# Optimization experiments

Measured on AMD Instinct MI355X. Metric: run time of the kernel, lower is better.

## Reference

```python
import jax, jax.numpy as jnp
import numpy as np

NUM_TERMS = 3
HIDDEN = 64
CLAMP_MIN = 1e-10


def _hermite_basis(x, num_terms):
    hs = [jnp.ones_like(x)]
    if num_terms > 1:
        hs.append(2.0 * x)
    for n in range(1, num_terms - 1):
        hs.append(2.0 * x * hs[n] - 2.0 * n * hs[n - 1])
    return jnp.stack(hs[:num_terms], axis=-1)  # (..., num_terms)


def setup_inputs() -> dict:
    key = jax.random.key(0)
    ks = jax.random.split(key, 7)
    B, S = 2048, 1024
    ys_coeffs = jax.random.normal(ks[0], (B, S, 2), dtype=jnp.float32)
    # scoring MLP params: Linear(3,64) -> ReLU -> Linear(64,64) -> ReLU -> Linear(64,num_terms)
    def lin(k, fan_in, fan_out):
        bound = 1.0 / np.sqrt(fan_in)
        kw, kb = jax.random.split(k)
        W = jax.random.uniform(kw, (fan_in, fan_out), minval=-bound, maxval=bound, dtype=jnp.float32)
        b = jax.random.uniform(kb, (fan_out,), minval=-bound, maxval=bound, dtype=jnp.float32)
        return W, b
    W1, b1 = lin(ks[1], 3, HIDDEN)
    W2, b2 = lin(ks[2], HIDDEN, HIDDEN)
    Wout, bout = lin(ks[3], HIDDEN, NUM_TERMS)
    return {"ys_coeffs": ys_coeffs, "W1": W1, "b1": b1, "W2": W2, "b2": b2,
            "Wout": Wout, "bout": bout}


def reference(ys_coeffs, W1, b1, W2, b2, Wout, bout):
    B, S, _ = ys_coeffs.shape
    timestamps = ys_coeffs[:, :, 0]
    values = ys_coeffs[:, :, 1]
    x0 = values[:, :-1]            # (B, S-1)
    xt = values[:, 1:]             # (B, S-1)
    t = timestamps[:, 1:]          # (B, S-1)
    feats = jnp.stack([xt, t, x0], axis=-1)           # (B, S-1, 3)
    h1 = jax.nn.relu(feats @ W1 + b1)                 # (B, S-1, 64)
    h2 = jax.nn.relu(h1 @ W2 + b2)                    # (B, S-1, 64)
    c_n = h2 @ Wout + bout                            # (B, S-1, num_terms)
    herm = _hermite_basis(xt, NUM_TERMS)              # (B, S-1, num_terms)
    p = jnp.sum(c_n * herm, axis=-1)                  # (B, S-1)
    p = jax.nn.softmax(p, axis=0)                     # softmax over batch dim (as in torch dim=0)
    log_likelihood = jnp.log(jnp.clip(p, CLAMP_MIN)).sum(axis=-1)  # (B,)
    return log_likelihood.mean()
```

## Files before the change

### kernel.cpp

```cpp
#include <hip/hip_runtime.h>
#include <hip/hip_bf16.h>

#define HIDDEN 64
#define BATCH 2048
#define SFULL 1024
#define SM1 1023
#define LN_CLAMP -23.025850929940457f
#define SP_PER 16

typedef __bf16 bf16x8 __attribute__((ext_vector_type(8)));
typedef float  f32x4  __attribute__((ext_vector_type(4)));
typedef float  f32x16 __attribute__((ext_vector_type(16)));
typedef short  s16x2  __attribute__((ext_vector_type(2)));

#define FRAG_UNITS 16

__device__ __forceinline__ int sig(int rg) {
    return 16 * ((rg >> 3) & 3) + 8 * ((rg >> 2) & 1) + (rg & 3) + 4 * (rg >> 5);
}

__device__ __forceinline__ unsigned pkt(float lo, float hi) {
    return __builtin_amdgcn_perm(__float_as_uint(hi), __float_as_uint(lo), 0x07060302u);
}
__device__ __forceinline__ unsigned rp(unsigned x) {
    s16x2 v = __builtin_bit_cast(s16x2, x);
    s16x2 z = {0, 0};
    v = __builtin_elementwise_max(v, z);
    return __builtin_bit_cast(unsigned, v);
}

__device__ __forceinline__ void relu_pack4(const f32x16 lo, const f32x16 hi, bf16x8* out) {
#pragma unroll
    for (int c = 0; c < 4; ++c) {
        union { unsigned u[4]; bf16x8 v; } r;
        r.u[0] = rp(pkt(lo[4 * c + 0], lo[4 * c + 1]));
        r.u[1] = rp(pkt(lo[4 * c + 2], lo[4 * c + 3]));
        r.u[2] = rp(pkt(hi[4 * c + 0], hi[4 * c + 1]));
        r.u[3] = rp(pkt(hi[4 * c + 2], hi[4 * c + 3]));
        out[c] = r.v;
    }
}

__device__ __forceinline__ bf16x8 featpk(float xt, float t, float x0) {
    union { unsigned u[4]; bf16x8 v; } r;
    r.u[0] = pkt(xt, t);
    r.u[1] = pkt(x0, 1.0f);
    r.u[2] = r.u[0]; r.u[3] = r.u[1];
    return r.v;
}

__global__ __launch_bounds__(256) void frag_setup_kernel(
    const float* __restrict__ W1, const float* __restrict__ b1,
    const float* __restrict__ W2, const float* __restrict__ b2,
    const float* __restrict__ Wout, char* __restrict__ F)
{
    const int l    = threadIdx.x & 63;
    const int wv   = threadIdx.x >> 6;
    const int pcol = l & 31;
    const int hi   = l >> 5;

    if (wv == 0) {
#pragma unroll
        for (int mt = 0; mt < 2; ++mt) {
            const int hout = sig(32 * mt + pcol);
            bf16x8 v;
#pragma unroll
            for (int j = 0; j < 8; ++j) {
                const int k = 8 * hi + j;
                v[j] = (k < 3) ? (__bf16)W1[k * 64 + hout]
                     : (k == 3) ? (__bf16)b1[hout] : (__bf16)0.0f;
            }
            *(bf16x8*)(F + ((mt * 64 + l) << 4)) = v;
        }
#pragma unroll
        for (int c = 0; c < 4; ++c) {
            bf16x8 v;
#pragma unroll
            for (int j = 0; j < 8; ++j) {
                const int k = 16 * c + 8 * hi + j;
                v[j] = (pcol < 3) ? (__bf16)Wout[k * 3 + pcol] : (__bf16)0.0f;
            }
            *(bf16x8*)(F + (((10 + c) * 64 + l) << 4)) = v;
        }
    } else if (wv == 1 || wv == 2) {
        const int mt = wv - 1;
        const int hout = sig(32 * mt + pcol);
#pragma unroll
        for (int c = 0; c < 4; ++c) {
            bf16x8 v;
#pragma unroll
            for (int j = 0; j < 8; ++j)
                v[j] = (__bf16)W2[(16 * c + 8 * hi + j) * 64 + hout];
            *(bf16x8*)(F + (((2 + mt * 4 + c) * 64 + l) << 4)) = v;
        }
    } else {
#pragma unroll
        for (int mt = 0; mt < 2; ++mt) {
            const int hout = sig(32 * mt + pcol);
            bf16x8 v;
#pragma unroll
            for (int j = 0; j < 8; ++j)
                v[j] = (hi == 0 && j == 0) ? (__bf16)b2[hout] : (__bf16)0.0f;
            *(bf16x8*)(F + (((14 + mt) * 64 + l) << 4)) = v;
        }
    }
}

__global__ __launch_bounds__(256, 4) void mlp_z_kernel(
    const float* __restrict__ ys,
    const char* __restrict__ F,
    const float* __restrict__ bout,
    float* __restrict__ z)
{
    __shared__ __align__(16) char Flds[14 * 64 * 16];

    const int l    = threadIdx.x & 63;
    const int wv   = threadIdx.x >> 6;
    const int pcol = l & 31;
    const int hi   = l >> 5;

    for (int i = threadIdx.x; i < 14 * 64; i += 256)
        *(f32x4*)(Flds + ((size_t)i << 4)) =
            *(const f32x4*)(F + ((size_t)(2 * 64 + i) << 4));

    const int b   = (blockIdx.x * 4 + wv) * 32 + pcol;
    const int sp0 = blockIdx.y * SP_PER;
    const int omax = (SFULL - 1) - sp0;

    bf16x8 a1r[2];
    a1r[0] = *(const bf16x8*)(F + ((0 * 64 + l) << 4));
    a1r[1] = *(const bf16x8*)(F + ((1 * 64 + l) << 4));

    bf16x8 Bone;
    {
        union { unsigned u[4]; bf16x8 v; } r;
        r.u[0] = (hi == 0) ? 0x3F80u : 0u;
        r.u[1] = 0u; r.u[2] = 0u; r.u[3] = 0u;
        Bone = r.v;
    }

    const float bo0 = bout[0], bo1 = bout[1], bo2 = bout[2];

    f32x16 zero16;
#pragma unroll
    for (int i = 0; i < 16; ++i) zero16[i] = 0.0f;

    const float2* base2 = reinterpret_cast<const float2*>(ys) + ((size_t)b * SFULL + sp0);
    float* zb = z + (size_t)sp0 * BATCH + b;

    float2 q0 = base2[0];
    float2 q1 = base2[min(1, omax)];
    float2 qn = base2[min(2, omax)];

    __syncthreads();

    for (int it = 0; it < SP_PER; ++it) {
        unsigned loff = (unsigned)(l << 4);
        asm volatile("" : "+v"(loff));
#define LDSF(u) (*(const bf16x8*)(Flds + ((u) * 1024) + loff))

        const float2 qn2 = base2[min(it + 3, omax)];

        const float x0 = q0.y, t = q1.x, xt = q1.y;
        const bf16x8 f0 = featpk(xt, t, x0);

        f32x16 acc1_0 = __builtin_amdgcn_mfma_f32_32x32x16_bf16(a1r[0], f0, zero16, 0, 0, 0);
        f32x16 acc1_1 = __builtin_amdgcn_mfma_f32_32x32x16_bf16(a1r[1], f0, zero16, 0, 0, 0);

        bf16x8 wb0 = LDSF(12), wb1 = LDSF(13);
        bf16x8 w2_0 = LDSF(0), w2_1 = LDSF(4);

        bf16x8 h1f[4];
        relu_pack4(acc1_0, acc1_1, h1f);

        f32x16 acc2_0 = __builtin_amdgcn_mfma_f32_32x32x16_bf16(wb0, Bone, zero16, 0, 0, 0);
        f32x16 acc2_1 = __builtin_amdgcn_mfma_f32_32x32x16_bf16(wb1, Bone, zero16, 0, 0, 0);

#pragma unroll
        for (int c = 0; c < 4; ++c) {
            bf16x8 n0, n1;
            if (c < 3) { n0 = LDSF(c + 1); n1 = LDSF(4 + c + 1); }
            acc2_0 = __builtin_amdgcn_mfma_f32_32x32x16_bf16(w2_0, h1f[c], acc2_0, 0, 0, 0);
            acc2_1 = __builtin_amdgcn_mfma_f32_32x32x16_bf16(w2_1, h1f[c], acc2_1, 0, 0, 0);
            if (c < 3) { w2_0 = n0; w2_1 = n1; }
        }

        bf16x8 h2f[4];
        relu_pack4(acc2_0, acc2_1, h2f);

        bf16x8 w3 = LDSF(8);
        f32x16 acc3;
#pragma unroll
        for (int c = 0; c < 4; ++c) {
            bf16x8 n3;
            if (c < 3) n3 = LDSF(8 + c + 1);
            acc3 = __builtin_amdgcn_mfma_f32_32x32x16_bf16(w3, h2f[c],
                        (c == 0) ? zero16 : acc3, 0, 0, 0);
            if (c < 3) w3 = n3;
        }
#undef LDSF

        const float c0 = acc3[0] + bo0;
        const float c1 = acc3[1] + bo1;
        const float c2 = acc3[2] + bo2;
        const float zv = fmaf(c2, fmaf(4.0f * xt, xt, -2.0f), fmaf(c1, xt + xt, c0));

        if (l < 32 && sp0 + it < SM1)
            zb[(size_t)it * BATCH] = zv;

        q0 = q1; q1 = qn; qn = qn2;
    }
}

__device__ __forceinline__ float blk_reduce_max(float v) {
    __shared__ float s[4];
#pragma unroll
    for (int off = 32; off >= 1; off >>= 1) v = fmaxf(v, __shfl_xor(v, off));
    if ((threadIdx.x & 63) == 0) s[threadIdx.x >> 6] = v;
    __syncthreads();
    v = fmaxf(fmaxf(s[0], s[1]), fmaxf(s[2], s[3]));
    __syncthreads();
    return v;
}

__device__ __forceinline__ float blk_reduce_sum(float v) {
    __shared__ float s[4];
#pragma unroll
    for (int off = 32; off >= 1; off >>= 1) v += __shfl_xor(v, off);
    if ((threadIdx.x & 63) == 0) s[threadIdx.x >> 6] = v;
    __syncthreads();
    v = (s[0] + s[1]) + (s[2] + s[3]);
    __syncthreads();
    return v;
}

__global__ __launch_bounds__(256) void col_softmax_kernel(
    const float* __restrict__ z, float* __restrict__ colsum)
{
    const int sp = blockIdx.x;
    const int tid = threadIdx.x;
    const float* col = z + (size_t)sp * BATCH;

    float vals[8];
    float m = -3.4e38f;
#pragma unroll
    for (int i = 0; i < 8; ++i) {
        vals[i] = col[tid + 256 * i];
        m = fmaxf(m, vals[i]);
    }
    const float M = blk_reduce_max(m);

    float se = 0.0f;
#pragma unroll
    for (int i = 0; i < 8; ++i) se += __expf(vals[i] - M);
    const float S = blk_reduce_sum(se);
    const float L = __logf(S);

    float acc = 0.0f;
#pragma unroll
    for (int i = 0; i < 8; ++i) acc += fmaxf(vals[i] - M - L, LN_CLAMP);
    const float T = blk_reduce_sum(acc);
    if (tid == 0) colsum[sp] = T;
}

__global__ __launch_bounds__(256) void final_reduce_kernel(
    const float* __restrict__ colsum, float* __restrict__ out)
{
    const int tid = threadIdx.x;
    float v = 0.0f;
    for (int i = tid; i < SM1; i += 256) v += colsum[i];
    const float T = blk_reduce_sum(v);
    if (tid == 0) out[0] = T / (float)BATCH;
}

extern "C" void kernel_launch(void* const* d_in, const int* in_sizes, int n_in,
                              void* d_out, int out_size, void* d_ws, size_t ws_size,
                              hipStream_t stream) {
    const float* ys   = (const float*)d_in[0];
    const float* W1   = (const float*)d_in[1];
    const float* b1   = (const float*)d_in[2];
    const float* W2   = (const float*)d_in[3];
    const float* b2   = (const float*)d_in[4];
    const float* Wout = (const float*)d_in[5];
    const float* bout = (const float*)d_in[6];
    float* out = (float*)d_out;

    float* z      = (float*)d_ws;
    float* colsum = z + (size_t)SM1 * BATCH;
    size_t fo = ((size_t)SM1 * BATCH + SM1) * sizeof(float);
    fo = (fo + 15) & ~(size_t)15;
    char* F = (char*)d_ws + fo;

    frag_setup_kernel<<<1, 256, 0, stream>>>(W1, b1, W2, b2, Wout, F);
    dim3 grid1(16, 64);
    mlp_z_kernel<<<grid1, 256, 0, stream>>>(ys, F, bout, z);
    col_softmax_kernel<<<SM1, 256, 0, stream>>>(z, colsum);
    final_reduce_kernel<<<1, 256, 0, stream>>>(colsum, out);
}
```

Before: 44.17 us.

## Software-pipeline layer-1 MFMA across timesteps and split layer-3 accumulation chain

Restructures the per-timestep loop into pairs with ping-pong accumulators, so the first-layer MFMA for the next timestep is issued while the current timestep runs layers 2 and 3. Layer 3 now uses two independent accumulator chains that are summed at the end, which shortens the dependent MFMA chain. Launch bounds drop from 4 to 2 blocks per CU to make room for the extra live accumulators. This trades occupancy for instruction-level parallelism inside each wave.

```diff
diff --git a/kernel.cpp b/kernel.cpp
--- a/kernel.cpp
+++ b/kernel.cpp
@@ -6,7 +6,7 @@
 #define SFULL 1024
 #define SM1 1023
 #define LN_CLAMP -23.025850929940457f
-#define SP_PER 16
+#define PAIRS 8
 
 typedef __bf16 bf16x8 __attribute__((ext_vector_type(8)));
 typedef float  f32x4  __attribute__((ext_vector_type(4)));
@@ -106,7 +106,7 @@
     }
 }
 
-__global__ __launch_bounds__(256, 4) void mlp_z_kernel(
+__global__ __launch_bounds__(256, 2) void mlp_z_kernel(
     const float* __restrict__ ys,
     const char* __restrict__ F,
     const float* __restrict__ bout,
@@ -124,7 +124,7 @@
             *(const f32x4*)(F + ((size_t)(2 * 64 + i) << 4));
 
     const int b   = (blockIdx.x * 4 + wv) * 32 + pcol;
-    const int sp0 = blockIdx.y * SP_PER;
+    const int sp0 = blockIdx.y * (2 * PAIRS);
     const int omax = (SFULL - 1) - sp0;
 
     bf16x8 a1r[2];
@@ -148,68 +148,74 @@
     const float2* base2 = reinterpret_cast<const float2*>(ys) + ((size_t)b * SFULL + sp0);
     float* zb = z + (size_t)sp0 * BATCH + b;
 
-    float2 q0 = base2[0];
-    float2 q1 = base2[min(1, omax)];
-    float2 qn = base2[min(2, omax)];
-
-    __syncthreads();
-
-    for (int it = 0; it < SP_PER; ++it) {
-        unsigned loff = (unsigned)(l << 4);
-        asm volatile("" : "+v"(loff));
+    float2 qa = base2[0];
+    float2 qb = base2[min(1, omax)];
+    float2 qc = base2[min(2, omax)];
+
+    __syncthreads();
+
+    f32x16 accP_0, accP_1, accQ_0, accQ_1;
+    {
+        const bf16x8 f0 = featpk(qb.y, qb.x, qa.y);
+        accP_0 = __builtin_amdgcn_mfma_f32_32x32x16_bf16(a1r[0], f0, zero16, 0, 0, 0);
+        accP_1 = __builtin_amdgcn_mfma_f32_32x32x16_bf16(a1r[1], f0, zero16, 0, 0, 0);
+    }
+
 #define LDSF(u) (*(const bf16x8*)(Flds + ((u) * 1024) + loff))
-
-        const float2 qn2 = base2[min(it + 3, omax)];
-
-        const float x0 = q0.y, t = q1.x, xt = q1.y;
-        const bf16x8 f0 = featpk(xt, t, x0);
-
-        f32x16 acc1_0 = __builtin_amdgcn_mfma_f32_32x32x16_bf16(a1r[0], f0, zero16, 0, 0, 0);
-        f32x16 acc1_1 = __builtin_amdgcn_mfma_f32_32x32x16_bf16(a1r[1], f0, zero16, 0, 0, 0);
-
-        bf16x8 wb0 = LDSF(12), wb1 = LDSF(13);
-        bf16x8 w2_0 = LDSF(0), w2_1 = LDSF(4);
-
-        bf16x8 h1f[4];
-        relu_pack4(acc1_0, acc1_1, h1f);
-
-        f32x16 acc2_0 = __builtin_amdgcn_mfma_f32_32x32x16_bf16(wb0, Bone, zero16, 0, 0, 0);
-        f32x16 acc2_1 = __builtin_amdgcn_mfma_f32_32x32x16_bf16(wb1, Bone, zero16, 0, 0, 0);
-
-#pragma unroll
-        for (int c = 0; c < 4; ++c) {
-            bf16x8 n0, n1;
-            if (c < 3) { n0 = LDSF(c + 1); n1 = LDSF(4 + c + 1); }
-            acc2_0 = __builtin_amdgcn_mfma_f32_32x32x16_bf16(w2_0, h1f[c], acc2_0, 0, 0, 0);
-            acc2_1 = __builtin_amdgcn_mfma_f32_32x32x16_bf16(w2_1, h1f[c], acc2_1, 0, 0, 0);
-            if (c < 3) { w2_0 = n0; w2_1 = n1; }
-        }
-
-        bf16x8 h2f[4];
-        relu_pack4(acc2_0, acc2_1, h2f);
-
-        bf16x8 w3 = LDSF(8);
-        f32x16 acc3;
-#pragma unroll
-        for (int c = 0; c < 4; ++c) {
-            bf16x8 n3;
-            if (c < 3) n3 = LDSF(8 + c + 1);
-            acc3 = __builtin_amdgcn_mfma_f32_32x32x16_bf16(w3, h2f[c],
-                        (c == 0) ? zero16 : acc3, 0, 0, 0);
-            if (c < 3) w3 = n3;
-        }
+#define BODY(ACC0, ACC1, NACC0, NACC1, XTCUR, F0NEXT, STORE_GUARD, ZOFF)        \
+    {                                                                           \
+        unsigned loff = (unsigned)(l << 4);                                     \
+        asm volatile("" : "+v"(loff));                                          \
+                         \
+        NACC0 = __builtin_amdgcn_mfma_f32_32x32x16_bf16(a1r[0], F0NEXT, zero16, 0, 0, 0); \
+        NACC1 = __builtin_amdgcn_mfma_f32_32x32x16_bf16(a1r[1], F0NEXT, zero16, 0, 0, 0); \
+                            \
+        bf16x8 wb0 = LDSF(12), wb1 = LDSF(13);                                  \
+        f32x16 acc2_0 = __builtin_amdgcn_mfma_f32_32x32x16_bf16(wb0, Bone, zero16, 0, 0, 0); \
+        f32x16 acc2_1 = __builtin_amdgcn_mfma_f32_32x32x16_bf16(wb1, Bone, zero16, 0, 0, 0); \
+        bf16x8 w2_0 = LDSF(0), w2_1 = LDSF(4);                                  \
+                          \
+        bf16x8 h1f[4];                                                          \
+        relu_pack4(ACC0, ACC1, h1f);                                            \
+        _Pragma("unroll")                                                       \
+        for (int c = 0; c < 4; ++c) {                                           \
+            bf16x8 n0, n1;                                                      \
+            if (c < 3) { n0 = LDSF(c + 1); n1 = LDSF(4 + c + 1); }              \
+            acc2_0 = __builtin_amdgcn_mfma_f32_32x32x16_bf16(w2_0, h1f[c], acc2_0, 0, 0, 0); \
+            acc2_1 = __builtin_amdgcn_mfma_f32_32x32x16_bf16(w2_1, h1f[c], acc2_1, 0, 0, 0); \
+            if (c < 3) { w2_0 = n0; w2_1 = n1; }                                \
+        }                                                                       \
+        bf16x8 h2f[4];                                                          \
+        relu_pack4(acc2_0, acc2_1, h2f);                                        \
+        bf16x8 w30 = LDSF(8), w31 = LDSF(9), w32 = LDSF(10), w33 = LDSF(11);    \
+                                   \
+        f32x16 acc3a = __builtin_amdgcn_mfma_f32_32x32x16_bf16(w30, h2f[0], zero16, 0, 0, 0); \
+        f32x16 acc3b = __builtin_amdgcn_mfma_f32_32x32x16_bf16(w32, h2f[2], zero16, 0, 0, 0); \
+        acc3a = __builtin_amdgcn_mfma_f32_32x32x16_bf16(w31, h2f[1], acc3a, 0, 0, 0); \
+        acc3b = __builtin_amdgcn_mfma_f32_32x32x16_bf16(w33, h2f[3], acc3b, 0, 0, 0); \
+        const float c0 = acc3a[0] + acc3b[0] + bo0;                             \
+        const float c1 = acc3a[1] + acc3b[1] + bo1;                             \
+        const float c2 = acc3a[2] + acc3b[2] + bo2;                             \
+        const float xt_ = (XTCUR);                                              \
+        const float zv = fmaf(c2, fmaf(4.0f * xt_, xt_, -2.0f),                 \
+                         fmaf(c1, xt_ + xt_, c0));                              \
+        if (l < 32 && (STORE_GUARD)) zb[(size_t)(ZOFF) * BATCH] = zv;           \
+    }
+
+    for (int it = 0; it < PAIRS; ++it) {
+        const bf16x8 f0b = featpk(qc.y, qc.x, qb.y);
+        const float2 nb = base2[min(2 * it + 3, omax)];
+        BODY(accP_0, accP_1, accQ_0, accQ_1, qb.y, f0b, true, 2 * it)
+
+        const bf16x8 f0c = featpk(nb.y, nb.x, qc.y);
+        const float2 nc = base2[min(2 * it + 4, omax)];
+        BODY(accQ_0, accQ_1, accP_0, accP_1, qc.y, f0c,
+             (sp0 + 2 * it + 1 < SM1), 2 * it + 1)
+
+        qa = qc; qb = nb; qc = nc;
+    }
+#undef BODY
 #undef LDSF
-
-        const float c0 = acc3[0] + bo0;
-        const float c1 = acc3[1] + bo1;
-        const float c2 = acc3[2] + bo2;
-        const float zv = fmaf(c2, fmaf(4.0f * xt, xt, -2.0f), fmaf(c1, xt + xt, c0));
-
-        if (l < 32 && sp0 + it < SM1)
-            zb[(size_t)it * BATCH] = zv;
-
-        q0 = q1; q1 = qn; qn = qn2;
-    }
 }
 
 __device__ __forceinline__ float blk_reduce_max(float v) {
```

Result: faster. 43.11 us (-2.4%).
